# Kernel tuning notes

Measured on AMD Instinct MI355X. Metric: run time of the kernel, lower is better.

The kernel has to match this reference:

```python
import jax, jax.numpy as jnp
import numpy as np

N_NODES = 50000
N_EDGES = 800000
IN_CH = 128
HID = 48
HEADS = 2
HH = HID * HEADS  # 96
N_GRAPHS = 64
NEG_SLOPE = 0.2


def _gat_layer(x, src, dst, n, W, a_src, a_dst, b, heads, out_ch):
    # x: [N, in]; W: [in, heads*out]; a_src/a_dst: [heads, out]; b: [heads*out]
    h = (x @ W).reshape(n, heads, out_ch)              # [N, H, C]
    es = (h * a_src).sum(-1)                            # [N, H]
    ed = (h * a_dst).sum(-1)                            # [N, H]
    e = jax.nn.leaky_relu(es[src] + ed[dst], NEG_SLOPE)  # [E, H]
    m = jax.ops.segment_max(e, dst, num_segments=n)      # segment softmax (stable)
    p = jnp.exp(e - m[dst])
    denom = jax.ops.segment_sum(p, dst, num_segments=n)
    alpha = p / denom[dst]                               # [E, H]
    out = jax.ops.segment_sum(alpha[:, :, None] * h[src], dst, num_segments=n)
    return out.reshape(n, heads * out_ch) + b


def setup_inputs() -> dict:
    key = jax.random.key(0)
    ks = jax.random.split(key, 20)
    x = jax.random.normal(ks[0], (N_NODES, IN_CH), dtype=jnp.float32)
    edge_index = jax.random.randint(ks[1], (2, N_EDGES), 0, N_NODES, dtype=jnp.int64)
    edge_weight = jax.random.uniform(ks[2], (N_EDGES,), dtype=jnp.float32)
    batch = jnp.sort(jax.random.randint(ks[3], (N_NODES,), 0, N_GRAPHS, dtype=jnp.int64))
    s = 0.1
    params = {
        'W1': jax.random.normal(ks[4], (IN_CH, HH)) * s,
        'as1': jax.random.normal(ks[5], (HEADS, HID)) * s,
        'ad1': jax.random.normal(ks[6], (HEADS, HID)) * s,
        'b1': jnp.zeros((HH,), jnp.float32),
        'W2': jax.random.normal(ks[7], (HH, HH)) * s,
        'as2': jax.random.normal(ks[8], (1, HH)) * s,
        'ad2': jax.random.normal(ks[9], (1, HH)) * s,
        'b2': jnp.zeros((HH,), jnp.float32),
        'W3': jax.random.normal(ks[10], (HH, HH)) * s,
        'as3': jax.random.normal(ks[11], (1, HH)) * s,
        'ad3': jax.random.normal(ks[12], (1, HH)) * s,
        'b3': jnp.zeros((HH,), jnp.float32),
        'W4': jax.random.normal(ks[13], (HH, HH)) * s,
        'as4': jax.random.normal(ks[14], (1, HH)) * s,
        'ad4': jax.random.normal(ks[15], (1, HH)) * s,
        'b4': jnp.zeros((HH,), jnp.float32),
        'Wc': jax.random.normal(ks[16], (HH, 1)) * s,
        'bc': jnp.zeros((1,), jnp.float32),
    }
    return {'x': x, 'edge_index': edge_index, 'edge_weight': edge_weight,
            'batch': batch, **params}


def reference(x, edge_index, edge_weight, batch,
              W1, as1, ad1, b1, W2, as2, ad2, b2,
              W3, as3, ad3, b3, W4, as4, ad4, b4, Wc, bc):
    n = x.shape[0]
    loops = jnp.arange(n, dtype=edge_index.dtype)  # PyG GATConv add_self_loops=True
    src = jnp.concatenate([edge_index[0], loops])
    dst = jnp.concatenate([edge_index[1], loops])
    # edge_weight is ignored by GATConv when edge_dim=None (faithful to PyG)
    h = jax.nn.relu(_gat_layer(x, src, dst, n, W1, as1, ad1, b1, HEADS, HID))
    h = jax.nn.relu(_gat_layer(h, src, dst, n, W2, as2, ad2, b2, 1, HH))
    h = jax.nn.relu(_gat_layer(h, src, dst, n, W3, as3, ad3, b3, 1, HH))
    h = jax.nn.relu(_gat_layer(h, src, dst, n, W4, as4, ad4, b4, 1, HH))
    # global_mean_pool
    sums = jax.ops.segment_sum(h, batch, num_segments=N_GRAPHS)
    cnts = jax.ops.segment_sum(jnp.ones((n, 1), h.dtype), batch, num_segments=N_GRAPHS)
    pooled = sums / jnp.maximum(cnts, 1.0)
    return jax.nn.sigmoid(pooled @ Wc + bc)
```

## Files before the change

### kernel.cpp

```cpp
#include <hip/hip_runtime.h>
#include <hip/hip_bf16.h>

#define NN 50000
#define NE 800000
#define NG 64
#define NBUCK 256
#define BN 196
#define EPB 4096
#define HB 196
#define SMAX 4200

typedef __attribute__((ext_vector_type(8))) short short8;
typedef __attribute__((ext_vector_type(4))) float float4v;
typedef __attribute__((ext_vector_type(2))) float float2v;

__device__ __forceinline__ float bf2f(unsigned short u){
    unsigned v = ((unsigned)u) << 16; float f; __builtin_memcpy(&f, &v, 4); return f;
}
__device__ __forceinline__ unsigned short f2bf(float f){
    unsigned u; __builtin_memcpy(&u, &f, 4);
    u = (u + 0x7fffu + ((u >> 16) & 1u)) >> 16;
    return (unsigned short)u;
}
__device__ __forceinline__ float lrelu(float v){ return v > 0.f ? v : 0.2f * v; }

__device__ __forceinline__ float ldflex(const void* p, long i, int isbf){
    if (isbf) return bf2f(((const unsigned short*)p)[i]);
    return ((const float*)p)[i];
}
__device__ __forceinline__ int ldidx(const int* p, long i, int is64){
    return p[is64 ? (i << 1) : i];
}

__device__ __forceinline__ unsigned int enc_fp8_1(float f){
    unsigned u; __builtin_memcpy(&u, &f, 4);
    unsigned s = (u >> 24) & 0x80u;
    float a = fabsf(f); a = fminf(a, 448.f);
    float x = a * 0x1p-120f;
    unsigned xu; __builtin_memcpy(&xu, &x, 4);
    unsigned r = (xu + 0x7FFFFu + ((xu >> 20) & 1u)) >> 20;
    if (r > 0x7Eu) r = 0x7Eu;
    return s | r;
}
__device__ __forceinline__ unsigned short pk_fp8(float a, float b){
#if __has_builtin(__builtin_amdgcn_cvt_pk_fp8_f32)
    int r = __builtin_amdgcn_cvt_pk_fp8_f32(a, b, 0, false);
    return (unsigned short)(r & 0xFFFF);
#else
    return (unsigned short)(enc_fp8_1(a) | (enc_fp8_1(b) << 8));
#endif
}
__device__ __forceinline__ float dec_fp8_manual(unsigned int byte){
    unsigned bits = ((byte & 0x80u) << 24) | ((byte & 0x7Fu) << 20);
    float f; __builtin_memcpy(&f, &bits, 4);
    return f * 0x1p120f;
}
__device__ __forceinline__ void dec_fp8x4_pk(unsigned int v, float2v& lo, float2v& hi){
#if __has_builtin(__builtin_amdgcn_cvt_pk_f32_fp8)
    lo = __builtin_amdgcn_cvt_pk_f32_fp8((int)v, false);
    hi = __builtin_amdgcn_cvt_pk_f32_fp8((int)v, true);
#else
    lo[0] = dec_fp8_manual(v & 0xFF);
    lo[1] = dec_fp8_manual((v >> 8) & 0xFF);
    hi[0] = dec_fp8_manual((v >> 16) & 0xFF);
    hi[1] = dec_fp8_manual((v >> 24) & 0xFF);
#endif
}

__device__ __forceinline__ float rdlane_f(float v, int l){
    int i; __builtin_memcpy(&i, &v, 4);
    int r = __builtin_amdgcn_readlane(i, l);
    float f; __builtin_memcpy(&f, &r, 4);
    return f;
}

__global__ void detect_kernel(const unsigned short* xu, const unsigned int* eiu,
                              const unsigned int* bu, int* flags, int* bcnt,
                              int* bcur, float* pooled, int* gcnt){
    if (blockIdx.x == 1){
        int tid = threadIdx.x;
        bcnt[tid] = 0;
        bcur[tid] = 0;
        for (int i = tid; i < NG * 96; i += 256) pooled[i] = 0.f;
        if (tid < NG) gcnt[tid] = 0;
        return;
    }
    if (threadIdx.x != 0) return;
    int hit = 0;
    for (int i = 0; i < 128; i++){
        int ex = (xu[2 * i] >> 7) & 0xFF;
        if (ex >= 100 && ex <= 140) hit++;
    }
    flags[0] = (hit >= 64) ? 1 : 0;
    int z = 0;
    for (int i = 0; i < 128; i++) if (eiu[2 * i + 1] == 0) z++;
    flags[1] = (z >= 120) ? 1 : 0;
    z = 0;
    for (int i = 0; i < 128; i++) if (bu[49745 + 2 * i] == 0) z++;
    flags[2] = (z >= 120) ? 1 : 0;
}

__global__ __launch_bounds__(256) void wtprep_kernel(const void* W0, const void* W1,
                                                     const void* W2, const void* W3,
                                                     unsigned short* wt_all,
                                                     const int* flags){
    int l = blockIdx.x;
    const void* W = (l == 0) ? W0 : (l == 1) ? W1 : (l == 2) ? W2 : W3;
    int K = (l == 0) ? 128 : 96;
    unsigned short* out = wt_all + ((l == 0) ? 0 : (96 * 128 + (l - 1) * 96 * 96));
    int isbf = flags[0];
    int tot = 96 * K;
    for (int i = threadIdx.x; i < tot; i += 256){
        int c = i / K, k = i - c * K;
        out[i] = f2bf(ldflex(W, (long)k * 96 + c, isbf));
    }
}

__global__ __launch_bounds__(256) void bhist_kernel(const int* __restrict__ ei,
                                                    int* __restrict__ bcnt,
                                                    const int* __restrict__ flags){
    __shared__ int h[NBUCK];
    int tid = threadIdx.x;
    h[tid] = 0; __syncthreads();
    int f64 = flags[1];
    long e0 = (long)blockIdx.x * EPB + tid;
    #pragma unroll
    for (int r = 0; r < 16; r++){
        long e = e0 + r * 256;
        if (e < NE){
            int d = ldidx(ei, NE + e, f64);
            atomicAdd(&h[d / BN], 1);
        }
    }
    __syncthreads();
    atomicAdd(&bcnt[tid], h[tid]);
}

__global__ __launch_bounds__(256) void bscatter_kernel(const int* __restrict__ ei,
                                                       const int* __restrict__ bcnt,
                                                       int* __restrict__ bcur,
                                                       int2* __restrict__ ebuf,
                                                       const int* __restrict__ flags){
    __shared__ int h[NBUCK], lofs[NBUCK], gbase[NBUCK], lcur[NBUCK], bb[NBUCK];
    __shared__ int2 lstage[EPB];
    int tid = threadIdx.x;
    int f64 = flags[1];
    {
        int v = bcnt[tid];
        bb[tid] = v; __syncthreads();
        for (int off = 1; off < 256; off <<= 1){
            int x = bb[tid];
            int y = (tid >= off) ? bb[tid - off] : 0;
            __syncthreads();
            bb[tid] = x + y;
            __syncthreads();
        }
        bb[tid] -= v;
    }
    h[tid] = 0; __syncthreads();
    int2 ed[16]; int bk[16];
    long e0 = (long)blockIdx.x * EPB + tid;
    #pragma unroll
    for (int r = 0; r < 16; r++){
        long e = e0 + r * 256;
        if (e < NE){
            int s = ldidx(ei, e, f64);
            int d = ldidx(ei, NE + e, f64);
            ed[r] = make_int2(s, d);
            bk[r] = d / BN;
            atomicAdd(&h[bk[r]], 1);
        } else bk[r] = -1;
    }
    __syncthreads();
    int v = h[tid];
    lofs[tid] = v; __syncthreads();
    for (int off = 1; off < 256; off <<= 1){
        int x = lofs[tid];
        int y = (tid >= off) ? lofs[tid - off] : 0;
        __syncthreads();
        lofs[tid] = x + y;
        __syncthreads();
    }
    int excl = lofs[tid] - v;
    lofs[tid] = excl;
    lcur[tid] = excl;
    if (v > 0) gbase[tid] = bb[tid] + atomicAdd(&bcur[tid], v);
    __syncthreads();
    #pragma unroll
    for (int r = 0; r < 16; r++){
        if (bk[r] >= 0){
            int p = atomicAdd(&lcur[bk[r]], 1);
            lstage[p] = ed[r];
        }
    }
    __syncthreads();
    long base = (long)blockIdx.x * EPB;
    int cnt = (NE - base < EPB) ? (int)(NE - base) : EPB;
    for (int j = tid; j < cnt; j += 256){
        int2 e = lstage[j];
        int i = e.y / BN;
        ebuf[gbase[i] + j - lofs[i]] = e;
    }
}

__global__ __launch_bounds__(256) void place_kernel(const int2* __restrict__ ebuf,
                                                    const int* __restrict__ bcnt,
                                                    int* __restrict__ row_ptr,
                                                    int2* __restrict__ csr2){
    __shared__ int sb[NBUCK];
    __shared__ int nh[BN];
    __shared__ int nofs[256];
    __shared__ int lcur[BN];
    __shared__ int2 stage[SMAX];
    int k = blockIdx.x, tid = threadIdx.x;
    int n0 = k * BN;
    sb[tid] = bcnt[tid]; __syncthreads();
    for (int off = 1; off < 256; off <<= 1){
        int x = sb[tid];
        int y = (tid >= off) ? sb[tid - off] : 0;
        __syncthreads();
        sb[tid] = x + y;
        __syncthreads();
    }
    int seg0 = (k == 0) ? 0 : sb[k - 1];
    int len = sb[k] - seg0;
    for (int i = tid; i < BN; i += 256) nh[i] = 0;
    __syncthreads();
    for (int j = tid; j < len; j += 256){
        int2 e = ebuf[seg0 + j];
        atomicAdd(&nh[e.y - n0], 1);
    }
    __syncthreads();
    int v = (tid < BN) ? nh[tid] : 0;
    nofs[tid] = v; __syncthreads();
    for (int off = 1; off < 256; off <<= 1){
        int x = nofs[tid];
        int y = (tid >= off) ? nofs[tid - off] : 0;
        __syncthreads();
        nofs[tid] = x + y;
        __syncthreads();
    }
    int excl = nofs[tid] - v;
    if (tid < BN){
        lcur[tid] = excl;
        int node = n0 + tid;
        if (node < NN) row_ptr[node] = seg0 + excl;
    }
    if (k == NBUCK - 1 && tid == 0) row_ptr[NN] = NE;
    __syncthreads();
    if (len <= SMAX){
        for (int j = tid; j < len; j += 256){
            int2 e = ebuf[seg0 + j];
            int p = atomicAdd(&lcur[e.y - n0], 1);
            stage[p] = e;
        }
        __syncthreads();
        for (int j = tid; j < len; j += 256)
            csr2[seg0 + j] = stage[j];
    } else {
        for (int j = tid; j < len; j += 256){
            int2 e = ebuf[seg0 + j];
            int p = atomicAdd(&lcur[e.y - n0], 1);
            csr2[seg0 + p] = e;
        }
    }
}

template<int K, int H, bool L1>
__global__ __launch_bounds__(256) void gemm_mfma(const void* __restrict__ Ain,
                                                 const unsigned short* __restrict__ Wt,
                                                 const void* __restrict__ as_,
                                                 const void* __restrict__ ad_,
                                                 unsigned short* __restrict__ hq16,
                                                 float* __restrict__ es,
                                                 float* __restrict__ ed,
                                                 float* __restrict__ pself,
                                                 const int* __restrict__ flags){
    __shared__ union {
        struct { unsigned short xs[64 * 40]; unsigned short wt[96 * 40]; } s;
        float hs[64 * 104];
    } u;
    int tid = threadIdx.x;
    int row0 = blockIdx.x * 64;
    int lane = tid & 63, w = tid >> 6;
    int m = lane & 15, q = lane >> 4;
    int isbf = flags[0];
    float4v acc[6];
    #pragma unroll
    for (int ct = 0; ct < 6; ct++) acc[ct] = (float4v){0.f, 0.f, 0.f, 0.f};

    int sr = tid >> 2, kp = tid & 3;
    int rr = row0 + sr; if (rr >= NN) rr = NN - 1;

    for (int k0 = 0; k0 < K; k0 += 32){
        uint4 av;
        if (L1 && !isbf){
            const float* xf = (const float*)Ain + (size_t)rr * K + k0 + kp * 8;
            float4 f1 = *(const float4*)xf;
            float4 f2 = *(const float4*)(xf + 4);
            av.x = (unsigned)f2bf(f1.x) | ((unsigned)f2bf(f1.y) << 16);
            av.y = (unsigned)f2bf(f1.z) | ((unsigned)f2bf(f1.w) << 16);
            av.z = (unsigned)f2bf(f2.x) | ((unsigned)f2bf(f2.y) << 16);
            av.w = (unsigned)f2bf(f2.z) | ((unsigned)f2bf(f2.w) << 16);
        } else {
            av = *(const uint4*)((const unsigned short*)Ain + (size_t)rr * K + k0 + kp * 8);
        }
        *(uint4*)(u.s.xs + sr * 40 + kp * 8) = av;
        for (int i = tid; i < 96 * 4; i += 256){
            int c = i >> 2, kq = i & 3;
            *(uint4*)(u.s.wt + c * 40 + kq * 8) =
                *(const uint4*)(Wt + (size_t)c * K + k0 + kq * 8);
        }
        __syncthreads();
        short8 a = *(const short8*)(u.s.xs + (w * 16 + m) * 40 + q * 8);
        #pragma unroll
        for (int ct = 0; ct < 6; ct++){
            short8 b = *(const short8*)(u.s.wt + (ct * 16 + m) * 40 + q * 8);
            acc[ct] = __builtin_amdgcn_mfma_f32_16x16x32_bf16(a, b, acc[ct], 0, 0, 0);
        }
        __syncthreads();
    }

    #pragma unroll
    for (int ct = 0; ct < 6; ct++)
        #pragma unroll
        for (int r = 0; r < 4; r++)
            u.hs[(w * 16 + q * 4 + r) * 104 + ct * 16 + m] = acc[ct][r];
    __syncthreads();

    int rl = tid >> 2, part = tid & 3;
    int row = row0 + rl;
    float hv[24];
    #pragma unroll
    for (int jj = 0; jj < 6; jj++)
        *(float4v*)&hv[jj * 4] = *(const float4v*)&u.hs[rl * 104 + part * 24 + jj * 4];

    float pes = 0.f, ped = 0.f;
    #pragma unroll
    for (int i = 0; i < 24; i++){
        int c = part * 24 + i;
        pes += hv[i] * ldflex(as_, c, isbf);
        ped += hv[i] * ldflex(ad_, c, isbf);
    }
    pes += __shfl_xor(pes, 1); ped += __shfl_xor(ped, 1);
    if (H == 1){ pes += __shfl_xor(pes, 2); ped += __shfl_xor(ped, 2); }

    if (row < NN){
        if (part == 0){
            es[(long)row * H] = pes; ed[(long)row * H] = ped;
            pself[(long)row * H] = __expf(lrelu(pes + ped));
        }
        if (H == 2 && part == 2){
            es[(long)row * H + 1] = pes; ed[(long)row * H + 1] = ped;
            pself[(long)row * H + 1] = __expf(lrelu(pes + ped));
        }
        unsigned short wds[12];
        #pragma unroll
        for (int j = 0; j < 12; j++) wds[j] = pk_fp8(hv[2 * j], hv[2 * j + 1]);
        uint2* dst = (uint2*)hq16 + (long)row * 16 + part * 3;
        #pragma unroll
        for (int j2 = 0; j2 < 3; j2++){
            uint2 v;
            v.x = (unsigned)wds[4 * j2] | ((unsigned)wds[4 * j2 + 1] << 16);
            v.y = (unsigned)wds[4 * j2 + 2] | ((unsigned)wds[4 * j2 + 3] << 16);
            dst[j2] = v;
        }
    }
}

template<int H>
__global__ __launch_bounds__(256) void pexp_kernel(const float* __restrict__ es,
                                                   const float* __restrict__ ed,
                                                   const int2* __restrict__ csr2,
                                                   void* __restrict__ edata){
    int i = blockIdx.x * 256 + threadIdx.x;
    if (i >= NE) return;
    int2 e = csr2[i];
    unsigned s32 = (unsigned)e.x * 32u;
    if (H == 1){
        float p = __expf(lrelu(es[e.x] + ed[e.y]));
        ((uint2*)edata)[i] = make_uint2(s32, __float_as_uint(p));
    } else {
        float p0 = __expf(lrelu(es[2 * (long)e.x] + ed[2 * (long)e.y]));
        float p1 = __expf(lrelu(es[2 * (long)e.x + 1] + ed[2 * (long)e.y + 1]));
        ((uint4*)edata)[i] = make_uint4(s32, __float_as_uint(p0),
                                        __float_as_uint(p1), 0u);
    }
}

template<int H>
__global__ __launch_bounds__(256) void attn_kernel(const unsigned int* __restrict__ hq,
                                                   const void* __restrict__ edata,
                                                   const float* __restrict__ pself,
                                                   const int* __restrict__ row_ptr,
                                                   const void* __restrict__ bias,
                                                   unsigned int* __restrict__ outb,
                                                   const int* __restrict__ flags){
    int lane = threadIdx.x & 63;
    int d = blockIdx.x * 4 + (threadIdx.x >> 6);
    if (d >= NN) return;
    int isbf = flags[0];
    int beg = row_ptr[d], deg = row_ptr[d + 1] - beg;
    int g = lane / 12;
    int cl = lane - g * 12;
    int head = (H == 2) ? ((cl >= 6) ? 1 : 0) : 0;
    int m = lane - 48;

    int s_nxt = 0; float p0_nxt = 0.f, p1_nxt = 0.f;
    if (lane >= 48 && m < deg){
        if (H == 1){
            uint2 e = ((const uint2*)edata)[beg + m];
            s_nxt = (int)e.x; p0_nxt = __uint_as_float(e.y);
        } else {
            uint4 e = ((const uint4*)edata)[beg + m];
            s_nxt = (int)e.x; p0_nxt = __uint_as_float(e.y); p1_nxt = __uint_as_float(e.z);
        }
    }

    float2v acc[4];
    #pragma unroll
    for (int k = 0; k < 4; k++) acc[k] = (float2v){0.f, 0.f};
    float dn0 = 0.f, dn1 = 0.f;
    int cl2 = 2 * cl;

    for (int base = 0; base < deg; base += 16){
        int s_cur = s_nxt; float p0c = p0_nxt, p1c = p1_nxt;
        dn0 += p0c; dn1 += p1c;
        int nb = base + 16;
        s_nxt = 0; p0_nxt = 0.f; p1_nxt = 0.f;
        if (lane >= 48 && nb + m < deg){
            if (H == 1){
                uint2 e = ((const uint2*)edata)[beg + nb + m];
                s_nxt = (int)e.x; p0_nxt = __uint_as_float(e.y);
            } else {
                uint4 e = ((const uint4*)edata)[beg + nb + m];
                s_nxt = (int)e.x; p0_nxt = __uint_as_float(e.y); p1_nxt = __uint_as_float(e.z);
            }
        }
        int cnt = deg - base; if (cnt > 16) cnt = 16;
        int steps = (cnt + 3) >> 2;
        auto do_step = [&](int t){
            int idx = 48 + 4 * t + g;
            int s32 = __shfl(s_cur, idx);
            float p;
            if (H == 2){
                float p0 = __shfl(p0c, idx);
                float p1 = __shfl(p1c, idx);
                p = head ? p1 : p0;
            } else {
                p = __shfl(p0c, idx);
            }
            uint2 v = make_uint2(0u, 0u);
            if (lane < 48) v = *(const uint2*)(hq + (unsigned)s32 + cl2);
            float2v lo0, hi0, lo1, hi1;
            dec_fp8x4_pk(v.x, lo0, hi0);
            dec_fp8x4_pk(v.y, lo1, hi1);
            float2v p2 = {p, p};
            acc[0] += p2 * lo0; acc[1] += p2 * hi0;
            acc[2] += p2 * lo1; acc[3] += p2 * hi1;
        };
        if (steps == 4){
            do_step(0); do_step(1); do_step(2); do_step(3);
        } else {
            for (int t = 0; t < steps; t++) do_step(t);
        }
    }

    for (int off = 1; off < 16; off <<= 1){
        dn0 += __shfl_xor(dn0, off);
        if (H == 2) dn1 += __shfl_xor(dn1, off);
    }
    float dn0_t = rdlane_f(dn0, 48);
    float dn1_t = (H == 2) ? rdlane_f(dn1, 48) : dn0_t;

    float t8[8];
    #pragma unroll
    for (int k = 0; k < 4; k++){ t8[2 * k] = acc[k][0]; t8[2 * k + 1] = acc[k][1]; }
    #pragma unroll
    for (int k = 0; k < 8; k++) t8[k] += __shfl(t8[k], lane + 24);
    #pragma unroll
    for (int k = 0; k < 8; k++) t8[k] += __shfl(t8[k], lane + 12);

    if (lane < 12){
        float ps = pself[(long)d * H + head];
        float dn = (head ? dn1_t : dn0_t) + ps;
        uint2 v = *(const uint2*)(hq + (unsigned)d * 32u + cl2);
        float2v lo0, hi0, lo1, hi1;
        dec_fp8x4_pk(v.x, lo0, hi0);
        dec_fp8x4_pk(v.y, lo1, hi1);
        float f[8] = {lo0[0], lo0[1], hi0[0], hi0[1], lo1[0], lo1[1], hi1[0], hi1[1]};
        int c0 = 8 * cl;
        unsigned short ob[8];
        #pragma unroll
        for (int k = 0; k < 8; k++){
            float o = (t8[k] + ps * f[k]) / dn + ldflex(bias, c0 + k, isbf);
            ob[k] = f2bf(fmaxf(o, 0.f));
        }
        uint4 vv;
        vv.x = (unsigned)ob[0] | ((unsigned)ob[1] << 16);
        vv.y = (unsigned)ob[2] | ((unsigned)ob[3] << 16);
        vv.z = (unsigned)ob[4] | ((unsigned)ob[5] << 16);
        vv.w = (unsigned)ob[6] | ((unsigned)ob[7] << 16);
        ((uint4*)outb)[(long)d * 12 + cl] = vv;
    }
}

__global__ __launch_bounds__(64) void pool_kernel(const unsigned int* __restrict__ bufb,
                                                  const int* __restrict__ batch,
                                                  float* __restrict__ pooled,
                                                  int* __restrict__ gcnt,
                                                  const int* __restrict__ flags){
    int f64 = flags[2];
    int n0 = blockIdx.x * 32;
    if (n0 >= NN) return;
    int n1 = n0 + 32; if (n1 > NN) n1 = NN;
    int lane = threadIdx.x;
    if (lane < 48){
        float a0 = 0.f, a1 = 0.f;
        int curg = ldidx(batch, n0, f64);
        for (int nd = n0; nd < n1; nd++){
            int g = ldidx(batch, nd, f64);
            if (g != curg){
                atomicAdd(&pooled[curg * 96 + 2 * lane], a0);
                atomicAdd(&pooled[curg * 96 + 2 * lane + 1], a1);
                a0 = a1 = 0.f; curg = g;
            }
            unsigned v = bufb[(long)nd * 48 + lane];
            a0 += bf2f((unsigned short)v);
            a1 += bf2f((unsigned short)(v >> 16));
        }
        atomicAdd(&pooled[curg * 96 + 2 * lane], a0);
        atomicAdd(&pooled[curg * 96 + 2 * lane + 1], a1);
    } else if (lane == 48){
        int cnt = 0;
        int curg = ldidx(batch, n0, f64);
        for (int nd = n0; nd < n1; nd++){
            int g = ldidx(batch, nd, f64);
            if (g != curg){
                atomicAdd(&gcnt[curg], cnt);
                cnt = 0; curg = g;
            }
            cnt++;
        }
        atomicAdd(&gcnt[curg], cnt);
    }
}

__global__ void final_kernel(const float* __restrict__ pooled, const int* __restrict__ gcnt,
                             const void* __restrict__ Wc, const void* __restrict__ bc,
                             void* __restrict__ outp, const int* __restrict__ flags){
    int isbf = flags[0];
    int g = threadIdx.x;
    if (g >= NG) return;
    float cnt = (float)gcnt[g];
    if (cnt < 1.f) cnt = 1.f;
    float acc = 0.f;
    for (int c = 0; c < 96; c++)
        acc += (pooled[g * 96 + c] / cnt) * ldflex(Wc, c, isbf);
    acc += ldflex(bc, 0, isbf);
    float sg = 1.f / (1.f + __expf(-acc));
    if (isbf) ((unsigned short*)outp)[g] = f2bf(sg);
    else      ((float*)outp)[g] = sg;
}

extern "C" void kernel_launch(void* const* d_in, const int* in_sizes, int n_in,
                              void* d_out, int out_size, void* d_ws, size_t ws_size,
                              hipStream_t stream){
    const void* x     = d_in[0];
    const int* ei     = (const int*)d_in[1];
    const int* batch  = (const int*)d_in[3];
    const void* W[4]  = {d_in[4],  d_in[8],  d_in[12], d_in[16]};
    const void* AS[4] = {d_in[5],  d_in[9],  d_in[13], d_in[17]};
    const void* AD[4] = {d_in[6],  d_in[10], d_in[14], d_in[18]};
    const void* B[4]  = {d_in[7],  d_in[11], d_in[15], d_in[19]};
    const void* Wc    = d_in[20];
    const void* bc    = d_in[21];

    char* p = (char*)d_ws;
    auto alloc = [&](size_t bytes) -> void* {
        void* r = (void*)p;
        p += (bytes + 255) & ~(size_t)255;
        return r;
    };
    int* flags     = (int*)alloc(16);
    unsigned int* hq = (unsigned int*)alloc((size_t)NN * 128);
    unsigned int* buf1b = (unsigned int*)alloc((size_t)NN * 96 * 2);
    void* edata    = alloc((size_t)NE * 16);
    unsigned short* wt_all = (unsigned short*)alloc((size_t)(96 * 128 + 3 * 96 * 96) * 2);
    float* es      = (float*)alloc((size_t)NN * 2 * 4);
    float* ed      = (float*)alloc((size_t)NN * 2 * 4);
    float* pself   = (float*)alloc((size_t)NN * 2 * 4);
    int* row_ptr   = (int*)alloc((size_t)(NN + 1) * 4);
    int2* csr2     = (int2*)alloc((size_t)NE * 8);
    int2* ebuf     = (int2*)alloc((size_t)NE * 8);
    int* bcnt      = (int*)alloc((size_t)NBUCK * 4);
    int* bcur      = (int*)alloc((size_t)NBUCK * 4);
    float* pooled  = (float*)alloc((size_t)NG * 96 * 4);
    int* gcnt      = (int*)alloc((size_t)NG * 4);

    detect_kernel<<<2, 256, 0, stream>>>((const unsigned short*)x, (const unsigned int*)ei,
                                         (const unsigned int*)batch, flags, bcnt, bcur,
                                         pooled, gcnt);
    wtprep_kernel<<<4, 256, 0, stream>>>(W[0], W[1], W[2], W[3], wt_all, flags);

    bhist_kernel<<<HB, 256, 0, stream>>>(ei, bcnt, flags);
    bscatter_kernel<<<HB, 256, 0, stream>>>(ei, bcnt, bcur, ebuf, flags);
    place_kernel<<<NBUCK, 256, 0, stream>>>(ebuf, bcnt, row_ptr, csr2);

    const int GB = (NN + 63) / 64;
    const int AB = (NN + 3) / 4;
    const int EB = (NE + 255) / 256;
    unsigned short* wt1 = wt_all;
    unsigned short* wt2 = wt_all + 96 * 128;
    unsigned short* wt3 = wt2 + 96 * 96;
    unsigned short* wt4 = wt3 + 96 * 96;

    gemm_mfma<128, 2, true><<<GB, 256, 0, stream>>>(x, wt1, AS[0], AD[0],
                                                    (unsigned short*)hq, es, ed, pself, flags);
    pexp_kernel<2><<<EB, 256, 0, stream>>>(es, ed, csr2, edata);
    attn_kernel<2><<<AB, 256, 0, stream>>>(hq, edata, pself, row_ptr, B[0], buf1b, flags);
    unsigned short* wts[3] = {wt2, wt3, wt4};
    for (int l = 1; l < 4; l++){
        gemm_mfma<96, 1, false><<<GB, 256, 0, stream>>>(buf1b, wts[l - 1], AS[l], AD[l],
                                                        (unsigned short*)hq, es, ed, pself, flags);
        pexp_kernel<1><<<EB, 256, 0, stream>>>(es, ed, csr2, edata);
        attn_kernel<1><<<AB, 256, 0, stream>>>(hq, edata, pself, row_ptr, B[l], buf1b, flags);
    }

    pool_kernel<<<(NN + 31) / 32, 64, 0, stream>>>(buf1b, batch, pooled, gcnt, flags);
    final_kernel<<<1, 64, 0, stream>>>(pooled, gcnt, Wc, bc, d_out, flags);
}
```

Before: 430.8 us.

## Fuse edge exp computation into attention kernel and shrink CSR to source-only ints

New measurement: 414.9 us. -3.7%, faster.

```diff
diff --git a/kernel.cpp b/kernel.cpp
--- a/kernel.cpp
+++ b/kernel.cpp
@@ -206,12 +206,12 @@
 __global__ __launch_bounds__(256) void place_kernel(const int2* __restrict__ ebuf,
                                                     const int* __restrict__ bcnt,
                                                     int* __restrict__ row_ptr,
-                                                    int2* __restrict__ csr2){
+                                                    int* __restrict__ csr){
     __shared__ int sb[NBUCK];
     __shared__ int nh[BN];
     __shared__ int nofs[256];
     __shared__ int lcur[BN];
-    __shared__ int2 stage[SMAX];
+    __shared__ int stage[SMAX];
     int k = blockIdx.x, tid = threadIdx.x;
     int n0 = k * BN;
     sb[tid] = bcnt[tid]; __syncthreads();
@@ -252,16 +252,16 @@
         for (int j = tid; j < len; j += 256){
             int2 e = ebuf[seg0 + j];
             int p = atomicAdd(&lcur[e.y - n0], 1);
-            stage[p] = e;
+            stage[p] = e.x;
         }
         __syncthreads();
         for (int j = tid; j < len; j += 256)
-            csr2[seg0 + j] = stage[j];
+            csr[seg0 + j] = stage[j];
     } else {
         for (int j = tid; j < len; j += 256){
             int2 e = ebuf[seg0 + j];
             int p = atomicAdd(&lcur[e.y - n0], 1);
-            csr2[seg0 + p] = e;
+            csr[seg0 + p] = e.x;
         }
     }
 }
@@ -369,30 +369,12 @@
 }
 
 template<int H>
-__global__ __launch_bounds__(256) void pexp_kernel(const float* __restrict__ es,
+__global__ __launch_bounds__(256) void attn_kernel(const unsigned int* __restrict__ hq,
+                                                   const float* __restrict__ es,
                                                    const float* __restrict__ ed,
-                                                   const int2* __restrict__ csr2,
-                                                   void* __restrict__ edata){
-    int i = blockIdx.x * 256 + threadIdx.x;
-    if (i >= NE) return;
-    int2 e = csr2[i];
-    unsigned s32 = (unsigned)e.x * 32u;
-    if (H == 1){
-        float p = __expf(lrelu(es[e.x] + ed[e.y]));
-        ((uint2*)edata)[i] = make_uint2(s32, __float_as_uint(p));
-    } else {
-        float p0 = __expf(lrelu(es[2 * (long)e.x] + ed[2 * (long)e.y]));
-        float p1 = __expf(lrelu(es[2 * (long)e.x + 1] + ed[2 * (long)e.y + 1]));
-        ((uint4*)edata)[i] = make_uint4(s32, __float_as_uint(p0),
-                                        __float_as_uint(p1), 0u);
-    }
-}
-
-template<int H>
-__global__ __launch_bounds__(256) void attn_kernel(const unsigned int* __restrict__ hq,
-                                                   const void* __restrict__ edata,
                                                    const float* __restrict__ pself,
                                                    const int* __restrict__ row_ptr,
+                                                   const int* __restrict__ csr,
                                                    const void* __restrict__ bias,
                                                    unsigned int* __restrict__ outb,
                                                    const int* __restrict__ flags){
@@ -405,15 +387,19 @@
     int cl = lane - g * 12;
     int head = (H == 2) ? ((cl >= 6) ? 1 : 0) : 0;
     int m = lane - 48;
+    float edd0 = ed[(long)d * H];
+    float edd1 = (H == 2) ? ed[(long)d * H + 1] : edd0;
 
     int s_nxt = 0; float p0_nxt = 0.f, p1_nxt = 0.f;
     if (lane >= 48 && m < deg){
+        int s = csr[beg + m];
+        s_nxt = s * 32;
         if (H == 1){
-            uint2 e = ((const uint2*)edata)[beg + m];
-            s_nxt = (int)e.x; p0_nxt = __uint_as_float(e.y);
+            p0_nxt = __expf(lrelu(es[s] + edd0));
         } else {
-            uint4 e = ((const uint4*)edata)[beg + m];
-            s_nxt = (int)e.x; p0_nxt = __uint_as_float(e.y); p1_nxt = __uint_as_float(e.z);
+            float2 e2 = *(const float2*)&es[2 * (long)s];
+            p0_nxt = __expf(lrelu(e2.x + edd0));
+            p1_nxt = __expf(lrelu(e2.y + edd1));
         }
     }
 
@@ -429,12 +415,14 @@
         int nb = base + 16;
         s_nxt = 0; p0_nxt = 0.f; p1_nxt = 0.f;
         if (lane >= 48 && nb + m < deg){
+            int s = csr[beg + nb + m];
+            s_nxt = s * 32;
             if (H == 1){
-                uint2 e = ((const uint2*)edata)[beg + nb + m];
-                s_nxt = (int)e.x; p0_nxt = __uint_as_float(e.y);
+                p0_nxt = __expf(lrelu(es[s] + edd0));
             } else {
-                uint4 e = ((const uint4*)edata)[beg + nb + m];
-                s_nxt = (int)e.x; p0_nxt = __uint_as_float(e.y); p1_nxt = __uint_as_float(e.z);
+                float2 e2 = *(const float2*)&es[2 * (long)s];
+                p0_nxt = __expf(lrelu(e2.x + edd0));
+                p1_nxt = __expf(lrelu(e2.y + edd1));
             }
         }
         int cnt = deg - base; if (cnt > 16) cnt = 16;
@@ -585,13 +573,12 @@
     int* flags     = (int*)alloc(16);
     unsigned int* hq = (unsigned int*)alloc((size_t)NN * 128);
     unsigned int* buf1b = (unsigned int*)alloc((size_t)NN * 96 * 2);
-    void* edata    = alloc((size_t)NE * 16);
     unsigned short* wt_all = (unsigned short*)alloc((size_t)(96 * 128 + 3 * 96 * 96) * 2);
     float* es      = (float*)alloc((size_t)NN * 2 * 4);
     float* ed      = (float*)alloc((size_t)NN * 2 * 4);
     float* pself   = (float*)alloc((size_t)NN * 2 * 4);
     int* row_ptr   = (int*)alloc((size_t)(NN + 1) * 4);
-    int2* csr2     = (int2*)alloc((size_t)NE * 8);
+    int* csr       = (int*)alloc((size_t)NE * 4);
     int2* ebuf     = (int2*)alloc((size_t)NE * 8);
     int* bcnt      = (int*)alloc((size_t)NBUCK * 4);
     int* bcur      = (int*)alloc((size_t)NBUCK * 4);
@@ -605,11 +592,10 @@
 
     bhist_kernel<<<HB, 256, 0, stream>>>(ei, bcnt, flags);
     bscatter_kernel<<<HB, 256, 0, stream>>>(ei, bcnt, bcur, ebuf, flags);
-    place_kernel<<<NBUCK, 256, 0, stream>>>(ebuf, bcnt, row_ptr, csr2);
+    place_kernel<<<NBUCK, 256, 0, stream>>>(ebuf, bcnt, row_ptr, csr);
 
     const int GB = (NN + 63) / 64;
     const int AB = (NN + 3) / 4;
-    const int EB = (NE + 255) / 256;
     unsigned short* wt1 = wt_all;
     unsigned short* wt2 = wt_all + 96 * 128;
     unsigned short* wt3 = wt2 + 96 * 96;
@@ -617,14 +603,12 @@
 
     gemm_mfma<128, 2, true><<<GB, 256, 0, stream>>>(x, wt1, AS[0], AD[0],
                                                     (unsigned short*)hq, es, ed, pself, flags);
-    pexp_kernel<2><<<EB, 256, 0, stream>>>(es, ed, csr2, edata);
-    attn_kernel<2><<<AB, 256, 0, stream>>>(hq, edata, pself, row_ptr, B[0], buf1b, flags);
+    attn_kernel<2><<<AB, 256, 0, stream>>>(hq, es, ed, pself, row_ptr, csr, B[0], buf1b, flags);
     unsigned short* wts[3] = {wt2, wt3, wt4};
     for (int l = 1; l < 4; l++){
         gemm_mfma<96, 1, false><<<GB, 256, 0, stream>>>(buf1b, wts[l - 1], AS[l], AD[l],
                                                         (unsigned short*)hq, es, ed, pself, flags);
-        pexp_kernel<1><<<EB, 256, 0, stream>>>(es, ed, csr2, edata);
-        attn_kernel<1><<<AB, 256, 0, stream>>>(hq, edata, pself, row_ptr, B[l], buf1b, flags);
+        attn_kernel<1><<<AB, 256, 0, stream>>>(hq, es, ed, pself, row_ptr, csr, B[l], buf1b, flags);
     }
 
     pool_kernel<<<(NN + 31) / 32, 64, 0, stream>>>(buf1b, batch, pooled, gcnt, flags);
```
